# Optimization experiments

Hardware: AMD Instinct MI355X
Metric: run time of the kernel (lower is better)

## Reference

```python
import jax, jax.numpy as jnp
import numpy as np

B, L, D, H = 8, 1024, 512, 8
HD = D // H            # head_dim = 64
MAX_SEQ = 1024         # max_sequence_len
TEMP = 1.0


def setup_inputs() -> dict:
    key = jax.random.key(0)
    ks = jax.random.split(key, 9)
    w = lambda k, shape: jax.random.normal(k, shape, jnp.float32) * 0.02
    return {
        "x_q": jax.random.normal(ks[0], (B, L, D), jnp.float32),
        "x_k": jax.random.normal(ks[1], (B, L, D), jnp.float32),
        "x_v": jax.random.normal(ks[2], (B, L, D), jnp.float32),
        # causal mask: 1 where future (masked), 0 elsewhere; added as mask * -1e9
        "mask": jnp.triu(jnp.ones((L, L), jnp.float32), k=1),
        "Wq": w(ks[3], (D, D)), "bq": jnp.zeros((D,), jnp.float32),
        "Wk": w(ks[4], (D, D)), "bk": jnp.zeros((D,), jnp.float32),
        "Wv": w(ks[5], (D, D)), "bv": jnp.zeros((D,), jnp.float32),
        "Wo": w(ks[6], (D, D)), "bo": jnp.zeros((D,), jnp.float32),
        "rel_emb": w(ks[7], (MAX_SEQ, HD)),
    }


def _heads(x, W, b):
    # Dense + split heads: [B,L,D] -> [B,H,L,HD]
    y = x @ W + b
    Bx, Lx, _ = x.shape
    return y.reshape(Bx, Lx, H, HD).transpose(0, 2, 1, 3)


def reference(x_q, x_k, x_v, mask, Wq, bq, Wk, bk, Wv, bv, Wo, bo, rel_emb):
    Bx, Lq, Dx = x_q.shape
    Lk = x_k.shape[1]
    q = _heads(x_q, Wq, bq)   # [B,H,Lq,HD]
    k = _heads(x_k, Wk, bk)   # [B,H,Lk,HD]
    v = _heads(x_v, Wv, bv)   # [B,H,Lk,HD]

    scores = jnp.einsum('bhld,bhmd->bhlm', q, k)  # [B,H,Lq,Lk]

    # relative-position scores (Music Transformer skew trick)
    start = max(0, MAX_SEQ - Lq)
    E = rel_emb[start:]                              # [M,HD], M == Lq
    M = E.shape[0]
    rel = jnp.einsum('bhld,md->bhlm', q, E)          # [B,H,Lq,M]
    rel_mask = jnp.flip(jnp.tril(jnp.ones((Lq, M), jnp.float32)), axis=1)
    rel = rel * rel_mask
    # skew: pad one col on left, reshape swapping last two dims, drop first row
    padded = jnp.pad(rel, ((0, 0), (0, 0), (0, 0), (1, 0)))       # [B,H,Lq,M+1]
    skewed = padded.reshape(Bx, H, M + 1, Lq)[:, :, 1:, :]        # [B,H,M,Lq]
    skewed = skewed[:, :, :, :Lk]                                 # key_len <= query_len

    logits = (scores + skewed) / (jnp.sqrt(jnp.float32(HD)) * TEMP)
    logits = logits + mask * (-1e9)
    attn = jax.nn.softmax(logits, axis=-1)                        # [B,H,Lq,Lk]

    out = jnp.einsum('bhlm,bhmd->bhld', attn, v)                  # [B,H,Lq,HD]
    out = out.transpose(0, 2, 1, 3).reshape(Bx, Lq, Dx)
    out = out @ Wo + bo
    return out, attn
```

## Files before the change

### kernel.cpp

```cpp
#include <hip/hip_runtime.h>

typedef unsigned short u16;
typedef short bf8 __attribute__((ext_vector_type(8)));
typedef float f32x4 __attribute__((ext_vector_type(4)));

#define Bc 8
#define Hc 8
#define Lc 1024
#define Dc 512
#define HDc 64

__device__ __forceinline__ u16 f2bf(float f) {
    unsigned int x; __builtin_memcpy(&x, &f, 4);
    x = x + 0x7fffu + ((x >> 16) & 1u);
    return (u16)(x >> 16);
}
union S8 { bf8 v; u16 s[8]; };

__global__ __launch_bounds__(256) void relcvt(const float* __restrict__ src,
                                              u16* __restrict__ dst) {
    const int idx = blockIdx.x * 256 + threadIdx.x;
    const float4 v = *(const float4*)(src + (size_t)idx * 4);
    ushort4 o; o.x = f2bf(v.x); o.y = f2bf(v.y); o.z = f2bf(v.z); o.w = f2bf(v.w);
    *(ushort4*)(dst + (size_t)idx * 4) = o;
}

__global__ __launch_bounds__(256) void wtrans(
    const float* __restrict__ w0, const float* __restrict__ w1,
    const float* __restrict__ w2, const float* __restrict__ w3,
    u16* __restrict__ o0, u16* __restrict__ o1,
    u16* __restrict__ o2, u16* __restrict__ o3)
{
    const float* W; u16* O;
    switch (blockIdx.z) {
        case 0: W = w0; O = o0; break;
        case 1: W = w1; O = o1; break;
        case 2: W = w2; O = o2; break;
        default: W = w3; O = o3; break;
    }
    __shared__ float tile[64][65];
    const int t = threadIdx.x;
    const int k0 = blockIdx.x * 64, n0 = blockIdx.y * 64;
#pragma unroll
    for (int s = 0; s < 4; ++s) {
        const int idx = s * 256 + t;
        const int r = idx >> 4, c = (idx & 15) * 4;
        const float4 v = *(const float4*)(W + (size_t)(k0 + r) * Dc + n0 + c);
        tile[r][c] = v.x; tile[r][c + 1] = v.y; tile[r][c + 2] = v.z; tile[r][c + 3] = v.w;
    }
    __syncthreads();
#pragma unroll
    for (int s = 0; s < 2; ++s) {
        const int idx = s * 256 + t;
        const int rn = idx >> 3, ck = (idx & 7) * 8;
        S8 o;
#pragma unroll
        for (int u = 0; u < 8; ++u) o.s[u] = f2bf(tile[ck + u][rn]);
        *(bf8*)(O + (size_t)(n0 + rn) * Dc + k0 + ck) = o.v;
    }
}

__global__ __launch_bounds__(256) void gemm_mfma(
    const void* __restrict__ A, const u16* __restrict__ WT,
    const float* __restrict__ bias, void* __restrict__ Y,
    int aF32, int mode)
{
    __shared__ u16 As[128][72];
    __shared__ u16 Bs[64][72];

    const int t = threadIdx.x;
    const int w = t >> 6, lane = t & 63, quad = lane >> 4, l15 = lane & 15;
    const int m0 = blockIdx.x * 128, n0 = blockIdx.y * 64;

    f32x4 acc[2][4] = {};

    for (int k0 = 0; k0 < Dc; k0 += 64) {
#pragma unroll
        for (int s = 0; s < 4; ++s) {
            const int idx = s * 256 + t;
            const int r = idx >> 3, cb = (idx & 7) * 8;
            if (aF32) {
                const float* ap = (const float*)A + (size_t)(m0 + r) * Dc + k0 + cb;
                const float4 v0 = *(const float4*)ap;
                const float4 v1 = *(const float4*)(ap + 4);
                S8 o;
                o.s[0] = f2bf(v0.x); o.s[1] = f2bf(v0.y); o.s[2] = f2bf(v0.z); o.s[3] = f2bf(v0.w);
                o.s[4] = f2bf(v1.x); o.s[5] = f2bf(v1.y); o.s[6] = f2bf(v1.z); o.s[7] = f2bf(v1.w);
                *(bf8*)&As[r][cb] = o.v;
            } else {
                *(bf8*)&As[r][cb] = *(const bf8*)((const u16*)A + (size_t)(m0 + r) * Dc + k0 + cb);
            }
        }
#pragma unroll
        for (int s = 0; s < 2; ++s) {
            const int idx = s * 256 + t;
            const int r = idx >> 3, cb = (idx & 7) * 8;
            *(bf8*)&Bs[r][cb] = *(const bf8*)(WT + (size_t)(n0 + r) * Dc + k0 + cb);
        }
        __syncthreads();
#pragma unroll
        for (int ks = 0; ks < 2; ++ks) {
            const bf8 a0 = *(const bf8*)&As[w * 32 + l15][ks * 32 + quad * 8];
            const bf8 a1 = *(const bf8*)&As[w * 32 + 16 + l15][ks * 32 + quad * 8];
#pragma unroll
            for (int nt = 0; nt < 4; ++nt) {
                const bf8 b = *(const bf8*)&Bs[nt * 16 + l15][ks * 32 + quad * 8];
                acc[0][nt] = __builtin_amdgcn_mfma_f32_16x16x32_bf16(a0, b, acc[0][nt], 0, 0, 0);
                acc[1][nt] = __builtin_amdgcn_mfma_f32_16x16x32_bf16(a1, b, acc[1][nt], 0, 0, 0);
            }
        }
        __syncthreads();
    }

#pragma unroll
    for (int nt = 0; nt < 4; ++nt) {
        const int n = n0 + nt * 16 + l15;
        const float bv = bias[n];
#pragma unroll
        for (int mt = 0; mt < 2; ++mt) {
#pragma unroll
            for (int reg = 0; reg < 4; ++reg) {
                const int m = m0 + w * 32 + mt * 16 + quad * 4 + reg;
                const float val = acc[mt][nt][reg] + bv;
                if (mode == 0) {
                    ((float*)Y)[(size_t)m * Dc + n] = val;
                } else {
                    const int b = m >> 10, l = m & 1023;
                    const int h = n >> 6, hd = n & 63;
                    ((u16*)Y)[(((size_t)(b * Hc + h)) * Lc + l) * HDc + hd] = f2bf(val);
                }
            }
        }
    }
}

__global__ __launch_bounds__(256) void attn_mfma(
    const u16* __restrict__ q, const u16* __restrict__ k,
    const u16* __restrict__ v, const u16* __restrict__ rel,
    float* __restrict__ attn, u16* __restrict__ ows)
{
    __shared__ u16 kps[2][64][72];
    __shared__ u16 vst[2][64][72];
    __shared__ float rs[64][84];
    __shared__ float ls[64];

    const int bh = blockIdx.x;
    const int px = blockIdx.y;
    const int t = threadIdx.x;
    const int w = t >> 6, lane = t & 63, quad = lane >> 4, l15 = lane & 15;
    const int nt0 = 3 - w;
    const size_t qb = ((size_t)bh << 10);
    const int sr = t >> 3, scb = (t & 7) * 8;

    for (int seg = 0; seg < 2; ++seg) {
        const int it = seg ? (15 - px) : px;
        const int i0 = it * 64;

        __syncthreads();
        if (t < 64) ls[t] = 0.f;

        bf8 aq[2];
#pragma unroll
        for (int ks = 0; ks < 2; ++ks)
            aq[ks] = *(const bf8*)(q + (qb + i0 + w * 16 + l15) * HDc + ks * 32 + quad * 8);

        {
            const bf8 k0r = *(const bf8*)(k + (qb + sr) * HDc + scb);
            const bf8 k1r = *(const bf8*)(k + (qb + 32 + sr) * HDc + scb);
            *(bf8*)&kps[0][sr][scb] = k0r;
            *(bf8*)&kps[0][32 + sr][scb] = k1r;
        }
        int cur = 0;
        for (int jt = 0; jt <= it; ++jt) {
            const int j0 = jt * 64;
            const int mb = 960 - i0 + j0 + nt0 * 16;
            __syncthreads();
            const bool pf = (jt < it);
            bf8 kn0 = {}, kn1 = {};
            if (pf) {
                kn0 = *(const bf8*)(k + (qb + j0 + 64 + sr) * HDc + scb);
                kn1 = *(const bf8*)(k + (qb + j0 + 96 + sr) * HDc + scb);
            }

            f32x4 aS[4] = {}; f32x4 aR[5] = {};
#pragma unroll
            for (int ks = 0; ks < 2; ++ks) {
                const bf8 a = aq[ks];
#pragma unroll
                for (int nt = 0; nt < 4; ++nt) {
                    const bf8 b = *(const bf8*)&kps[cur][nt * 16 + l15][ks * 32 + quad * 8];
                    aS[nt] = __builtin_amdgcn_mfma_f32_16x16x32_bf16(a, b, aS[nt], 0, 0, 0);
                }
#pragma unroll
                for (int nt = 0; nt < 5; ++nt) {
                    int row = mb + nt * 16 + l15;
                    row = row > 1023 ? 1023 : row;
                    const bf8 b = *(const bf8*)(rel + (size_t)row * HDc + ks * 32 + quad * 8);
                    aR[nt] = __builtin_amdgcn_mfma_f32_16x16x32_bf16(a, b, aR[nt], 0, 0, 0);
                }
            }
#pragma unroll
            for (int nt = 0; nt < 5; ++nt)
#pragma unroll
                for (int reg = 0; reg < 4; ++reg)
                    rs[w * 16 + quad * 4 + reg][nt * 16 + l15] = aR[nt][reg];

            float psum[4] = {0.f, 0.f, 0.f, 0.f};
#pragma unroll
            for (int nt = 0; nt < 4; ++nt) {
#pragma unroll
                for (int reg = 0; reg < 4; ++reg) {
                    const int Rl = w * 16 + quad * 4 + reg;
                    const int cp = 15 - quad * 4 - reg + nt * 16 + l15;
                    const float sc = (aS[nt][reg] + rs[Rl][cp]) * 0.125f;
                    const bool valid = (j0 + nt * 16 + l15) <= (i0 + Rl);
                    psum[reg] += valid ? __expf(sc) : 0.f;
                }
            }
#pragma unroll
            for (int m = 1; m < 16; m <<= 1)
#pragma unroll
                for (int reg = 0; reg < 4; ++reg) psum[reg] += __shfl_xor(psum[reg], m, 64);
            if (l15 == 0) {
#pragma unroll
                for (int reg = 0; reg < 4; ++reg) ls[w * 16 + quad * 4 + reg] += psum[reg];
            }
            if (pf) {
                *(bf8*)&kps[cur ^ 1][sr][scb] = kn0;
                *(bf8*)&kps[cur ^ 1][32 + sr][scb] = kn1;
                cur ^= 1;
            }
        }

        __syncthreads();
        if (t < 64) ls[t] = 1.f / ls[t];

        f32x4 acc[4] = {};

        {
            const bf8 k0r = *(const bf8*)(k + (qb + sr) * HDc + scb);
            const bf8 k1r = *(const bf8*)(k + (qb + 32 + sr) * HDc + scb);
            S8 v0; v0.v = *(const bf8*)(v + (qb + sr) * HDc + scb);
            S8 v1; v1.v = *(const bf8*)(v + (qb + 32 + sr) * HDc + scb);
            *(bf8*)&kps[0][sr][scb] = k0r;
            *(bf8*)&kps[0][32 + sr][scb] = k1r;
            const int cp0 = (sr & 7) + 8 * (((sr >> 3) + (scb >> 3)) & 7);
            const int cp1 = (sr & 7) + 8 * ((4 + (sr >> 3) + (scb >> 3)) & 7);
#pragma unroll
            for (int u = 0; u < 8; ++u) vst[0][scb + u][cp0] = v0.s[u];
#pragma unroll
            for (int u = 0; u < 8; ++u) vst[0][scb + u][cp1] = v1.s[u];
        }
        cur = 0;
        for (int jt = 0; jt <= it; ++jt) {
            const int j0 = jt * 64;
            const int mb = 960 - i0 + j0 + nt0 * 16;
            __syncthreads();
            const bool pf = (jt < it);
            bf8 kn0 = {}, kn1 = {}, vn0 = {}, vn1 = {};
            if (pf) {
                kn0 = *(const bf8*)(k + (qb + j0 + 64 + sr) * HDc + scb);
                kn1 = *(const bf8*)(k + (qb + j0 + 96 + sr) * HDc + scb);
                vn0 = *(const bf8*)(v + (qb + j0 + 64 + sr) * HDc + scb);
                vn1 = *(const bf8*)(v + (qb + j0 + 96 + sr) * HDc + scb);
            }

            f32x4 aS[4] = {}; f32x4 aR[5] = {};
#pragma unroll
            for (int ks = 0; ks < 2; ++ks) {
                const bf8 a = aq[ks];
#pragma unroll
                for (int nt = 0; nt < 4; ++nt) {
                    const bf8 b = *(const bf8*)&kps[cur][nt * 16 + l15][ks * 32 + quad * 8];
                    aS[nt] = __builtin_amdgcn_mfma_f32_16x16x32_bf16(a, b, aS[nt], 0, 0, 0);
                }
#pragma unroll
                for (int nt = 0; nt < 5; ++nt) {
                    int row = mb + nt * 16 + l15;
                    row = row > 1023 ? 1023 : row;
                    const bf8 b = *(const bf8*)(rel + (size_t)row * HDc + ks * 32 + quad * 8);
                    aR[nt] = __builtin_amdgcn_mfma_f32_16x16x32_bf16(a, b, aR[nt], 0, 0, 0);
                }
            }
#pragma unroll
            for (int nt = 0; nt < 5; ++nt)
#pragma unroll
                for (int reg = 0; reg < 4; ++reg)
                    rs[w * 16 + quad * 4 + reg][nt * 16 + l15] = aR[nt][reg];

#pragma unroll
            for (int nt = 0; nt < 4; ++nt) {
                float pvv[4];
#pragma unroll
                for (int reg = 0; reg < 4; ++reg) {
                    const int Rl = w * 16 + quad * 4 + reg;
                    const int cp = 15 - quad * 4 - reg + nt * 16 + l15;
                    const float sc = (aS[nt][reg] + rs[Rl][cp]) * 0.125f;
                    const bool valid = (j0 + nt * 16 + l15) <= (i0 + Rl);
                    pvv[reg] = valid ? __expf(sc) * ls[Rl] : 0.f;
                }
                asm volatile("" ::: "memory");
#pragma unroll
                for (int reg = 0; reg < 4; ++reg) {
                    const int Rl = w * 16 + quad * 4 + reg;
                    attn[((size_t)bh * Lc + i0 + Rl) * Lc + j0 + nt * 16 + l15] = pvv[reg];
                    ((u16*)&rs[Rl][0])[nt * 16 + l15] = f2bf(pvv[reg]);
                }
            }

#pragma unroll
            for (int ks = 0; ks < 2; ++ks) {
                const bf8 pa = *(const bf8*)((const u16*)&rs[w * 16 + l15][0] + ks * 32 + quad * 8);
#pragma unroll
                for (int nt = 0; nt < 4; ++nt) {
                    const int d = nt * 16 + l15;
                    const bf8 vb = *(const bf8*)&vst[cur][d][8 * (((ks * 4 + quad) + (d >> 3)) & 7)];
                    acc[nt] = __builtin_amdgcn_mfma_f32_16x16x32_bf16(pa, vb, acc[nt], 0, 0, 0);
                }
            }

            if (pf) {
                *(bf8*)&kps[cur ^ 1][sr][scb] = kn0;
                *(bf8*)&kps[cur ^ 1][32 + sr][scb] = kn1;
                S8 a0; a0.v = vn0; S8 a1; a1.v = vn1;
                const int cp0 = (sr & 7) + 8 * (((sr >> 3) + (scb >> 3)) & 7);
                const int cp1 = (sr & 7) + 8 * ((4 + (sr >> 3) + (scb >> 3)) & 7);
#pragma unroll
                for (int u = 0; u < 8; ++u) vst[cur ^ 1][scb + u][cp0] = a0.s[u];
#pragma unroll
                for (int u = 0; u < 8; ++u) vst[cur ^ 1][scb + u][cp1] = a1.s[u];
                cur ^= 1;
            }
        }

        const int bb = bh >> 3, hh = bh & 7;
#pragma unroll
        for (int nt = 0; nt < 4; ++nt)
#pragma unroll
            for (int reg = 0; reg < 4; ++reg)
                ows[((size_t)(bb * Lc + i0 + w * 16 + quad * 4 + reg)) * Dc + hh * HDc + nt * 16 + l15]
                    = f2bf(acc[nt][reg]);

        const int jend = (it + 1) * 64;
        if (jend + t * 4 < Lc) {
            const float4 z = make_float4(0.f, 0.f, 0.f, 0.f);
            for (int r = 0; r < 64; ++r)
                *(float4*)(attn + ((size_t)bh * Lc + i0 + r) * Lc + jend + t * 4) = z;
        }
    }
}

extern "C" void kernel_launch(void* const* d_in, const int* in_sizes, int n_in,
                              void* d_out, int out_size, void* d_ws, size_t ws_size,
                              hipStream_t stream)
{
    const float* x_q = (const float*)d_in[0];
    const float* x_k = (const float*)d_in[1];
    const float* x_v = (const float*)d_in[2];
    const float* Wq = (const float*)d_in[4];
    const float* bq = (const float*)d_in[5];
    const float* Wk = (const float*)d_in[6];
    const float* bk = (const float*)d_in[7];
    const float* Wv = (const float*)d_in[8];
    const float* bv = (const float*)d_in[9];
    const float* Wo = (const float*)d_in[10];
    const float* bo = (const float*)d_in[11];
    const float* rel = (const float*)d_in[12];

    float* out  = (float*)d_out;
    float* attn = out + (size_t)Bc * Lc * Dc;

    u16* relbf = (u16*)d_ws;
    u16* wqT = relbf + (size_t)1024 * 64;
    u16* wkT = wqT + (size_t)Dc * Dc;
    u16* wvT = wkT + (size_t)Dc * Dc;
    u16* woT = wvT + (size_t)Dc * Dc;
    u16* qbf = woT + (size_t)Dc * Dc;
    u16* kbf = qbf + (size_t)Bc * Lc * Dc;
    u16* vbf = kbf + (size_t)Bc * Lc * Dc;
    u16* owsbf = vbf + (size_t)Bc * Lc * Dc;

    relcvt<<<64, 256, 0, stream>>>(rel, relbf);
    wtrans<<<dim3(8, 8, 4), 256, 0, stream>>>(Wq, Wk, Wv, Wo, wqT, wkT, wvT, woT);

    dim3 gg(64, 8);
    gemm_mfma<<<gg, 256, 0, stream>>>(x_q, wqT, bq, qbf, 1, 1);
    gemm_mfma<<<gg, 256, 0, stream>>>(x_k, wkT, bk, kbf, 1, 1);
    gemm_mfma<<<gg, 256, 0, stream>>>(x_v, wvT, bv, vbf, 1, 1);

    attn_mfma<<<dim3(64, 8), 256, 0, stream>>>(qbf, kbf, vbf, relbf, attn, owsbf);

    gemm_mfma<<<gg, 256, 0, stream>>>(owsbf, woT, bo, out, 0, 0);
}
```

Before: 549.1 us.

## Double-buffer GEMM with XCD-aware tiling and coalesced nontemporal attention stores

```diff
diff --git a/kernel.cpp b/kernel.cpp
--- a/kernel.cpp
+++ b/kernel.cpp
@@ -65,51 +65,81 @@
     const float* __restrict__ bias, void* __restrict__ Y,
     int aF32, int mode)
 {
-    __shared__ u16 As[128][72];
-    __shared__ u16 Bs[64][72];
+    __shared__ u16 As[2][64][72];
+    __shared__ u16 Bs[2][64][72];
+
+    const int wgid = blockIdx.x;
+    const int xcd = wgid & 7, rr = wgid >> 3;
+    const int mt = xcd + 8 * (rr >> 3), ntile = rr & 7;
+    const int m0 = mt * 64, n0 = ntile * 64;
 
     const int t = threadIdx.x;
     const int w = t >> 6, lane = t & 63, quad = lane >> 4, l15 = lane & 15;
-    const int m0 = blockIdx.x * 128, n0 = blockIdx.y * 64;
-
-    f32x4 acc[2][4] = {};
-
+    const int ra = t >> 2, ca = (t & 3) * 16;
+
+    f32x4 acc[4] = {};
+
+    {
+        S8 o0, o1;
+        if (aF32) {
+            const float* ap = (const float*)A + (size_t)(m0 + ra) * Dc + ca;
+            const float4 v0 = *(const float4*)ap,       v1 = *(const float4*)(ap + 4);
+            const float4 v2 = *(const float4*)(ap + 8), v3 = *(const float4*)(ap + 12);
+            o0.s[0] = f2bf(v0.x); o0.s[1] = f2bf(v0.y); o0.s[2] = f2bf(v0.z); o0.s[3] = f2bf(v0.w);
+            o0.s[4] = f2bf(v1.x); o0.s[5] = f2bf(v1.y); o0.s[6] = f2bf(v1.z); o0.s[7] = f2bf(v1.w);
+            o1.s[0] = f2bf(v2.x); o1.s[1] = f2bf(v2.y); o1.s[2] = f2bf(v2.z); o1.s[3] = f2bf(v2.w);
+            o1.s[4] = f2bf(v3.x); o1.s[5] = f2bf(v3.y); o1.s[6] = f2bf(v3.z); o1.s[7] = f2bf(v3.w);
+        } else {
+            const u16* ap = (const u16*)A + (size_t)(m0 + ra) * Dc + ca;
+            o0.v = *(const bf8*)ap; o1.v = *(const bf8*)(ap + 8);
+        }
+        *(bf8*)&As[0][ra][ca] = o0.v; *(bf8*)&As[0][ra][ca + 8] = o1.v;
+        const u16* bp = WT + (size_t)(n0 + ra) * Dc + ca;
+        *(bf8*)&Bs[0][ra][ca] = *(const bf8*)bp;
+        *(bf8*)&Bs[0][ra][ca + 8] = *(const bf8*)(bp + 8);
+    }
+
+    int cur = 0;
     for (int k0 = 0; k0 < Dc; k0 += 64) {
-#pragma unroll
-        for (int s = 0; s < 4; ++s) {
-            const int idx = s * 256 + t;
-            const int r = idx >> 3, cb = (idx & 7) * 8;
+        __syncthreads();
+        const bool pf = (k0 + 64 < Dc);
+        float4 v0, v1, v2, v3; bf8 an0 = {}, an1 = {}, bn0 = {}, bn1 = {};
+        if (pf) {
+            const int kn = k0 + 64;
             if (aF32) {
-                const float* ap = (const float*)A + (size_t)(m0 + r) * Dc + k0 + cb;
-                const float4 v0 = *(const float4*)ap;
-                const float4 v1 = *(const float4*)(ap + 4);
-                S8 o;
-                o.s[0] = f2bf(v0.x); o.s[1] = f2bf(v0.y); o.s[2] = f2bf(v0.z); o.s[3] = f2bf(v0.w);
-                o.s[4] = f2bf(v1.x); o.s[5] = f2bf(v1.y); o.s[6] = f2bf(v1.z); o.s[7] = f2bf(v1.w);
-                *(bf8*)&As[r][cb] = o.v;
+                const float* ap = (const float*)A + (size_t)(m0 + ra) * Dc + kn + ca;
+                v0 = *(const float4*)ap;       v1 = *(const float4*)(ap + 4);
+                v2 = *(const float4*)(ap + 8); v3 = *(const float4*)(ap + 12);
             } else {
-                *(bf8*)&As[r][cb] = *(const bf8*)((const u16*)A + (size_t)(m0 + r) * Dc + k0 + cb);
-            }
-        }
-#pragma unroll
-        for (int s = 0; s < 2; ++s) {
-            const int idx = s * 256 + t;
-            const int r = idx >> 3, cb = (idx & 7) * 8;
-            *(bf8*)&Bs[r][cb] = *(const bf8*)(WT + (size_t)(n0 + r) * Dc + k0 + cb);
-        }
-        __syncthreads();
+                const u16* ap = (const u16*)A + (size_t)(m0 + ra) * Dc + kn + ca;
+                an0 = *(const bf8*)ap; an1 = *(const bf8*)(ap + 8);
+            }
+            const u16* bp = WT + (size_t)(n0 + ra) * Dc + kn + ca;
+            bn0 = *(const bf8*)bp; bn1 = *(const bf8*)(bp + 8);
+        }
+
 #pragma unroll
         for (int ks = 0; ks < 2; ++ks) {
-            const bf8 a0 = *(const bf8*)&As[w * 32 + l15][ks * 32 + quad * 8];
-            const bf8 a1 = *(const bf8*)&As[w * 32 + 16 + l15][ks * 32 + quad * 8];
+            const bf8 a = *(const bf8*)&As[cur][w * 16 + l15][ks * 32 + quad * 8];
 #pragma unroll
             for (int nt = 0; nt < 4; ++nt) {
-                const bf8 b = *(const bf8*)&Bs[nt * 16 + l15][ks * 32 + quad * 8];
-                acc[0][nt] = __builtin_amdgcn_mfma_f32_16x16x32_bf16(a0, b, acc[0][nt], 0, 0, 0);
-                acc[1][nt] = __builtin_amdgcn_mfma_f32_16x16x32_bf16(a1, b, acc[1][nt], 0, 0, 0);
-            }
-        }
-        __syncthreads();
+                const bf8 b = *(const bf8*)&Bs[cur][nt * 16 + l15][ks * 32 + quad * 8];
+                acc[nt] = __builtin_amdgcn_mfma_f32_16x16x32_bf16(a, b, acc[nt], 0, 0, 0);
+            }
+        }
+
+        if (pf) {
+            S8 o0, o1;
+            if (aF32) {
+                o0.s[0] = f2bf(v0.x); o0.s[1] = f2bf(v0.y); o0.s[2] = f2bf(v0.z); o0.s[3] = f2bf(v0.w);
+                o0.s[4] = f2bf(v1.x); o0.s[5] = f2bf(v1.y); o0.s[6] = f2bf(v1.z); o0.s[7] = f2bf(v1.w);
+                o1.s[0] = f2bf(v2.x); o1.s[1] = f2bf(v2.y); o1.s[2] = f2bf(v2.z); o1.s[3] = f2bf(v2.w);
+                o1.s[4] = f2bf(v3.x); o1.s[5] = f2bf(v3.y); o1.s[6] = f2bf(v3.z); o1.s[7] = f2bf(v3.w);
+            } else { o0.v = an0; o1.v = an1; }
+            *(bf8*)&As[cur ^ 1][ra][ca] = o0.v; *(bf8*)&As[cur ^ 1][ra][ca + 8] = o1.v;
+            *(bf8*)&Bs[cur ^ 1][ra][ca] = bn0;  *(bf8*)&Bs[cur ^ 1][ra][ca + 8] = bn1;
+            cur ^= 1;
+        }
     }
 
 #pragma unroll
@@ -117,18 +147,15 @@
         const int n = n0 + nt * 16 + l15;
         const float bv = bias[n];
 #pragma unroll
-        for (int mt = 0; mt < 2; ++mt) {
-#pragma unroll
-            for (int reg = 0; reg < 4; ++reg) {
-                const int m = m0 + w * 32 + mt * 16 + quad * 4 + reg;
-                const float val = acc[mt][nt][reg] + bv;
-                if (mode == 0) {
-                    ((float*)Y)[(size_t)m * Dc + n] = val;
-                } else {
-                    const int b = m >> 10, l = m & 1023;
-                    const int h = n >> 6, hd = n & 63;
-                    ((u16*)Y)[(((size_t)(b * Hc + h)) * Lc + l) * HDc + hd] = f2bf(val);
-                }
+        for (int reg = 0; reg < 4; ++reg) {
+            const int m = m0 + w * 16 + quad * 4 + reg;
+            const float val = acc[nt][reg] + bv;
+            if (mode == 0) {
+                __builtin_nontemporal_store(val, (float*)Y + (size_t)m * Dc + n);
+            } else {
+                const int b = m >> 10, l = m & 1023;
+                const int h = n >> 6, hd = n & 63;
+                ((u16*)Y)[(((size_t)(b * Hc + h)) * Lc + l) * HDc + hd] = f2bf(val);
             }
         }
     }
@@ -141,7 +168,7 @@
 {
     __shared__ u16 kps[2][64][72];
     __shared__ u16 vst[2][64][72];
-    __shared__ float rs[64][84];
+    __shared__ float rs[64][96];
     __shared__ float ls[64];
 
     const int bh = blockIdx.x;
@@ -288,23 +315,26 @@
                 for (int reg = 0; reg < 4; ++reg)
                     rs[w * 16 + quad * 4 + reg][nt * 16 + l15] = aR[nt][reg];
 
+            float pvv[4][4];
 #pragma unroll
             for (int nt = 0; nt < 4; ++nt) {
-                float pvv[4];
 #pragma unroll
                 for (int reg = 0; reg < 4; ++reg) {
                     const int Rl = w * 16 + quad * 4 + reg;
                     const int cp = 15 - quad * 4 - reg + nt * 16 + l15;
                     const float sc = (aS[nt][reg] + rs[Rl][cp]) * 0.125f;
                     const bool valid = (j0 + nt * 16 + l15) <= (i0 + Rl);
-                    pvv[reg] = valid ? __expf(sc) * ls[Rl] : 0.f;
-                }
-                asm volatile("" ::: "memory");
+                    pvv[nt][reg] = valid ? __expf(sc) * ls[Rl] : 0.f;
+                }
+            }
+            asm volatile("" ::: "memory");
+#pragma unroll
+            for (int nt = 0; nt < 4; ++nt) {
 #pragma unroll
                 for (int reg = 0; reg < 4; ++reg) {
                     const int Rl = w * 16 + quad * 4 + reg;
-                    attn[((size_t)bh * Lc + i0 + Rl) * Lc + j0 + nt * 16 + l15] = pvv[reg];
-                    ((u16*)&rs[Rl][0])[nt * 16 + l15] = f2bf(pvv[reg]);
+                    ((u16*)&rs[Rl][0])[nt * 16 + l15] = f2bf(pvv[nt][reg]);
+                    rs[Rl][32 + nt * 16 + l15] = pvv[nt][reg];
                 }
             }
 
@@ -331,6 +361,15 @@
                 for (int u = 0; u < 8; ++u) vst[cur ^ 1][scb + u][cp1] = a1.s[u];
                 cur ^= 1;
             }
+
+            __syncthreads();
+            const int trow = t >> 4, tcol = (t & 15) * 4;
+#pragma unroll
+            for (int s = 0; s < 4; ++s) {
+                const f32x4 p4 = *(const f32x4*)&rs[trow + 16 * s][32 + tcol];
+                __builtin_nontemporal_store(p4,
+                    (f32x4*)(attn + ((size_t)bh * Lc + i0 + trow + 16 * s) * Lc + j0 + tcol));
+            }
         }
 
         const int bb = bh >> 3, hh = bh & 7;
@@ -343,9 +382,10 @@
 
         const int jend = (it + 1) * 64;
         if (jend + t * 4 < Lc) {
-            const float4 z = make_float4(0.f, 0.f, 0.f, 0.f);
+            const f32x4 z = {0.f, 0.f, 0.f, 0.f};
             for (int r = 0; r < 64; ++r)
-                *(float4*)(attn + ((size_t)bh * Lc + i0 + r) * Lc + jend + t * 4) = z;
+                __builtin_nontemporal_store(z,
+                    (f32x4*)(attn + ((size_t)bh * Lc + i0 + r) * Lc + jend + t * 4));
         }
     }
 }
@@ -383,12 +423,11 @@
     relcvt<<<64, 256, 0, stream>>>(rel, relbf);
     wtrans<<<dim3(8, 8, 4), 256, 0, stream>>>(Wq, Wk, Wv, Wo, wqT, wkT, wvT, woT);
 
-    dim3 gg(64, 8);
-    gemm_mfma<<<gg, 256, 0, stream>>>(x_q, wqT, bq, qbf, 1, 1);
-    gemm_mfma<<<gg, 256, 0, stream>>>(x_k, wkT, bk, kbf, 1, 1);
-    gemm_mfma<<<gg, 256, 0, stream>>>(x_v, wvT, bv, vbf, 1, 1);
+    gemm_mfma<<<1024, 256, 0, stream>>>(x_q, wqT, bq, qbf, 1, 1);
+    gemm_mfma<<<1024, 256, 0, stream>>>(x_k, wkT, bk, kbf, 1, 1);
+    gemm_mfma<<<1024, 256, 0, stream>>>(x_v, wvT, bv, vbf, 1, 1);
 
     attn_mfma<<<dim3(64, 8), 256, 0, stream>>>(qbf, kbf, vbf, relbf, attn, owsbf);
 
-    gemm_mfma<<<gg, 256, 0, stream>>>(owsbf, woT, bo, out, 0, 0);
-}
+    gemm_mfma<<<1024, 256, 0, stream>>>(owsbf, woT, bo, out, 0, 0);
+}
```

Measured after the change: 469.8 us. -14.4%, faster.

## Double-buffer GEMM tiles, XCD-aware block mapping, shuffle-based rel skew, coalesced attn stores

Applied to the files above, without the earlier changes.

```diff
diff --git a/kernel.cpp b/kernel.cpp
--- a/kernel.cpp
+++ b/kernel.cpp
@@ -65,65 +65,111 @@
     const float* __restrict__ bias, void* __restrict__ Y,
     int aF32, int mode)
 {
-    __shared__ u16 As[128][72];
-    __shared__ u16 Bs[64][72];
+    __shared__ u16 As[2][128][72];
+    __shared__ u16 Bs[2][64][72];
+
+    const int wgid = blockIdx.x;
+    const int xcd = wgid & 7, rr = wgid >> 3;
+    const int mt = xcd * 8 + (rr >> 3), ntl = rr & 7;
+    const int m0 = mt * 128, n0 = ntl * 64;
 
     const int t = threadIdx.x;
     const int w = t >> 6, lane = t & 63, quad = lane >> 4, l15 = lane & 15;
-    const int m0 = blockIdx.x * 128, n0 = blockIdx.y * 64;
 
     f32x4 acc[2][4] = {};
 
-    for (int k0 = 0; k0 < Dc; k0 += 64) {
+    {
 #pragma unroll
         for (int s = 0; s < 4; ++s) {
-            const int idx = s * 256 + t;
-            const int r = idx >> 3, cb = (idx & 7) * 8;
+            const int idx = s * 256 + t, r = idx >> 3, cb = (idx & 7) * 8;
+            S8 o;
             if (aF32) {
-                const float* ap = (const float*)A + (size_t)(m0 + r) * Dc + k0 + cb;
-                const float4 v0 = *(const float4*)ap;
-                const float4 v1 = *(const float4*)(ap + 4);
-                S8 o;
+                const float* ap = (const float*)A + (size_t)(m0 + r) * Dc + cb;
+                const float4 v0 = *(const float4*)ap, v1 = *(const float4*)(ap + 4);
                 o.s[0] = f2bf(v0.x); o.s[1] = f2bf(v0.y); o.s[2] = f2bf(v0.z); o.s[3] = f2bf(v0.w);
                 o.s[4] = f2bf(v1.x); o.s[5] = f2bf(v1.y); o.s[6] = f2bf(v1.z); o.s[7] = f2bf(v1.w);
-                *(bf8*)&As[r][cb] = o.v;
             } else {
-                *(bf8*)&As[r][cb] = *(const bf8*)((const u16*)A + (size_t)(m0 + r) * Dc + k0 + cb);
-            }
+                o.v = *(const bf8*)((const u16*)A + (size_t)(m0 + r) * Dc + cb);
+            }
+            *(bf8*)&As[0][r][cb] = o.v;
         }
 #pragma unroll
         for (int s = 0; s < 2; ++s) {
-            const int idx = s * 256 + t;
-            const int r = idx >> 3, cb = (idx & 7) * 8;
-            *(bf8*)&Bs[r][cb] = *(const bf8*)(WT + (size_t)(n0 + r) * Dc + k0 + cb);
-        }
+            const int idx = s * 256 + t, r = idx >> 3, cb = (idx & 7) * 8;
+            *(bf8*)&Bs[0][r][cb] = *(const bf8*)(WT + (size_t)(n0 + r) * Dc + cb);
+        }
+    }
+
+    int cur = 0;
+    for (int k0 = 0; k0 < Dc; k0 += 64) {
         __syncthreads();
+        const bool pf = (k0 + 64 < Dc);
+        float4 fv[4][2]; bf8 av[4] = {}; bf8 bv[2] = {};
+        if (pf) {
+            const int kn = k0 + 64;
+#pragma unroll
+            for (int s = 0; s < 4; ++s) {
+                const int idx = s * 256 + t, r = idx >> 3, cb = (idx & 7) * 8;
+                if (aF32) {
+                    const float* ap = (const float*)A + (size_t)(m0 + r) * Dc + kn + cb;
+                    fv[s][0] = *(const float4*)ap; fv[s][1] = *(const float4*)(ap + 4);
+                } else {
+                    av[s] = *(const bf8*)((const u16*)A + (size_t)(m0 + r) * Dc + kn + cb);
+                }
+            }
+#pragma unroll
+            for (int s = 0; s < 2; ++s) {
+                const int idx = s * 256 + t, r = idx >> 3, cb = (idx & 7) * 8;
+                bv[s] = *(const bf8*)(WT + (size_t)(n0 + r) * Dc + kn + cb);
+            }
+        }
+
 #pragma unroll
         for (int ks = 0; ks < 2; ++ks) {
-            const bf8 a0 = *(const bf8*)&As[w * 32 + l15][ks * 32 + quad * 8];
-            const bf8 a1 = *(const bf8*)&As[w * 32 + 16 + l15][ks * 32 + quad * 8];
+            const bf8 a0 = *(const bf8*)&As[cur][w * 32 + l15][ks * 32 + quad * 8];
+            const bf8 a1 = *(const bf8*)&As[cur][w * 32 + 16 + l15][ks * 32 + quad * 8];
 #pragma unroll
             for (int nt = 0; nt < 4; ++nt) {
-                const bf8 b = *(const bf8*)&Bs[nt * 16 + l15][ks * 32 + quad * 8];
+                const bf8 b = *(const bf8*)&Bs[cur][nt * 16 + l15][ks * 32 + quad * 8];
                 acc[0][nt] = __builtin_amdgcn_mfma_f32_16x16x32_bf16(a0, b, acc[0][nt], 0, 0, 0);
                 acc[1][nt] = __builtin_amdgcn_mfma_f32_16x16x32_bf16(a1, b, acc[1][nt], 0, 0, 0);
             }
         }
-        __syncthreads();
+
+        if (pf) {
+#pragma unroll
+            for (int s = 0; s < 4; ++s) {
+                const int idx = s * 256 + t, r = idx >> 3, cb = (idx & 7) * 8;
+                S8 o;
+                if (aF32) {
+                    o.s[0] = f2bf(fv[s][0].x); o.s[1] = f2bf(fv[s][0].y);
+                    o.s[2] = f2bf(fv[s][0].z); o.s[3] = f2bf(fv[s][0].w);
+                    o.s[4] = f2bf(fv[s][1].x); o.s[5] = f2bf(fv[s][1].y);
+                    o.s[6] = f2bf(fv[s][1].z); o.s[7] = f2bf(fv[s][1].w);
+                } else { o.v = av[s]; }
+                *(bf8*)&As[cur ^ 1][r][cb] = o.v;
+            }
+#pragma unroll
+            for (int s = 0; s < 2; ++s) {
+                const int idx = s * 256 + t, r = idx >> 3, cb = (idx & 7) * 8;
+                *(bf8*)&Bs[cur ^ 1][r][cb] = bv[s];
+            }
+            cur ^= 1;
+        }
     }
 
 #pragma unroll
     for (int nt = 0; nt < 4; ++nt) {
         const int n = n0 + nt * 16 + l15;
-        const float bv = bias[n];
-#pragma unroll
-        for (int mt = 0; mt < 2; ++mt) {
+        const float bv2 = bias[n];
+#pragma unroll
+        for (int mi = 0; mi < 2; ++mi) {
 #pragma unroll
             for (int reg = 0; reg < 4; ++reg) {
-                const int m = m0 + w * 32 + mt * 16 + quad * 4 + reg;
-                const float val = acc[mt][nt][reg] + bv;
+                const int m = m0 + w * 32 + mi * 16 + quad * 4 + reg;
+                const float val = acc[mi][nt][reg] + bv2;
                 if (mode == 0) {
-                    ((float*)Y)[(size_t)m * Dc + n] = val;
+                    __builtin_nontemporal_store(val, (float*)Y + (size_t)m * Dc + n);
                 } else {
                     const int b = m >> 10, l = m & 1023;
                     const int h = n >> 6, hd = n & 63;
@@ -141,7 +187,8 @@
 {
     __shared__ u16 kps[2][64][72];
     __shared__ u16 vst[2][64][72];
-    __shared__ float rs[64][84];
+    __shared__ u16 p16[64][72];
+    __shared__ float p32[64][68];
     __shared__ float ls[64];
 
     const int bh = blockIdx.x;
@@ -151,6 +198,14 @@
     const int nt0 = 3 - w;
     const size_t qb = ((size_t)bh << 10);
     const int sr = t >> 3, scb = (t & 7) * 8;
+
+    int sl[4]; bool cy[4];
+#pragma unroll
+    for (int reg = 0; reg < 4; ++reg) {
+        const int s = l15 + 15 - (quad * 4 + reg);
+        sl[reg] = (quad << 4) | (s & 15);
+        cy[reg] = s >= 16;
+    }
 
     for (int seg = 0; seg < 2; ++seg) {
         const int it = seg ? (15 - px) : px;
@@ -199,11 +254,13 @@
                     aR[nt] = __builtin_amdgcn_mfma_f32_16x16x32_bf16(a, b, aR[nt], 0, 0, 0);
                 }
             }
-#pragma unroll
-            for (int nt = 0; nt < 5; ++nt)
+
+            float g[5][4];
+#pragma unroll
+            for (int m = 0; m < 5; ++m)
 #pragma unroll
                 for (int reg = 0; reg < 4; ++reg)
-                    rs[w * 16 + quad * 4 + reg][nt * 16 + l15] = aR[nt][reg];
+                    g[m][reg] = __shfl(aR[m][reg], sl[reg], 64);
 
             float psum[4] = {0.f, 0.f, 0.f, 0.f};
 #pragma unroll
@@ -211,8 +268,8 @@
 #pragma unroll
                 for (int reg = 0; reg < 4; ++reg) {
                     const int Rl = w * 16 + quad * 4 + reg;
-                    const int cp = 15 - quad * 4 - reg + nt * 16 + l15;
-                    const float sc = (aS[nt][reg] + rs[Rl][cp]) * 0.125f;
+                    const float relv = cy[reg] ? g[nt + 1][reg] : g[nt][reg];
+                    const float sc = (aS[nt][reg] + relv) * 0.125f;
                     const bool valid = (j0 + nt * 16 + l15) <= (i0 + Rl);
                     psum[reg] += valid ? __expf(sc) : 0.f;
                 }
@@ -282,35 +339,36 @@
                     aR[nt] = __builtin_amdgcn_mfma_f32_16x16x32_bf16(a, b, aR[nt], 0, 0, 0);
                 }
             }
-#pragma unroll
-            for (int nt = 0; nt < 5; ++nt)
+
+            float g[5][4];
+#pragma unroll
+            for (int m = 0; m < 5; ++m)
 #pragma unroll
                 for (int reg = 0; reg < 4; ++reg)
-                    rs[w * 16 + quad * 4 + reg][nt * 16 + l15] = aR[nt][reg];
+                    g[m][reg] = __shfl(aR[m][reg], sl[reg], 64);
+
+            float ils[4];
+#pragma unroll
+            for (int reg = 0; reg < 4; ++reg) ils[reg] = ls[w * 16 + quad * 4 + reg];
 
 #pragma unroll
             for (int nt = 0; nt < 4; ++nt) {
-                float pvv[4];
 #pragma unroll
                 for (int reg = 0; reg < 4; ++reg) {
                     const int Rl = w * 16 + quad * 4 + reg;
-                    const int cp = 15 - quad * 4 - reg + nt * 16 + l15;
-                    const float sc = (aS[nt][reg] + rs[Rl][cp]) * 0.125f;
+                    const float relv = cy[reg] ? g[nt + 1][reg] : g[nt][reg];
+                    const float sc = (aS[nt][reg] + relv) * 0.125f;
                     const bool valid = (j0 + nt * 16 + l15) <= (i0 + Rl);
-                    pvv[reg] = valid ? __expf(sc) * ls[Rl] : 0.f;
-                }
-                asm volatile("" ::: "memory");
-#pragma unroll
-                for (int reg = 0; reg < 4; ++reg) {
-                    const int Rl = w * 16 + quad * 4 + reg;
-                    attn[((size_t)bh * Lc + i0 + Rl) * Lc + j0 + nt * 16 + l15] = pvv[reg];
-                    ((u16*)&rs[Rl][0])[nt * 16 + l15] = f2bf(pvv[reg]);
-                }
-            }
+                    const float p = valid ? __expf(sc) * ils[reg] : 0.f;
+                    p16[Rl][nt * 16 + l15] = f2bf(p);
+                    p32[Rl][nt * 16 + l15] = p;
+                }
+            }
+            asm volatile("" ::: "memory");
 
 #pragma unroll
             for (int ks = 0; ks < 2; ++ks) {
-                const bf8 pa = *(const bf8*)((const u16*)&rs[w * 16 + l15][0] + ks * 32 + quad * 8);
+                const bf8 pa = *(const bf8*)((const u16*)&p16[w * 16 + l15][0] + ks * 32 + quad * 8);
 #pragma unroll
                 for (int nt = 0; nt < 4; ++nt) {
                     const int d = nt * 16 + l15;
@@ -331,6 +389,15 @@
                 for (int u = 0; u < 8; ++u) vst[cur ^ 1][scb + u][cp1] = a1.s[u];
                 cur ^= 1;
             }
+
+            __syncthreads();
+            const int trow = t >> 4, tcol = (t & 15) * 4;
+#pragma unroll
+            for (int s = 0; s < 4; ++s) {
+                const f32x4 p4 = *(const f32x4*)&p32[trow + 16 * s][tcol];
+                __builtin_nontemporal_store(p4,
+                    (f32x4*)(attn + ((size_t)bh * Lc + i0 + trow + 16 * s) * Lc + j0 + tcol));
+            }
         }
 
         const int bb = bh >> 3, hh = bh & 7;
@@ -343,9 +410,10 @@
 
         const int jend = (it + 1) * 64;
         if (jend + t * 4 < Lc) {
-            const float4 z = make_float4(0.f, 0.f, 0.f, 0.f);
+            const f32x4 z = {0.f, 0.f, 0.f, 0.f};
             for (int r = 0; r < 64; ++r)
-                *(float4*)(attn + ((size_t)bh * Lc + i0 + r) * Lc + jend + t * 4) = z;
+                __builtin_nontemporal_store(z,
+                    (f32x4*)(attn + ((size_t)bh * Lc + i0 + r) * Lc + jend + t * 4));
         }
     }
 }
@@ -383,12 +451,11 @@
     relcvt<<<64, 256, 0, stream>>>(rel, relbf);
     wtrans<<<dim3(8, 8, 4), 256, 0, stream>>>(Wq, Wk, Wv, Wo, wqT, wkT, wvT, woT);
 
-    dim3 gg(64, 8);
-    gemm_mfma<<<gg, 256, 0, stream>>>(x_q, wqT, bq, qbf, 1, 1);
-    gemm_mfma<<<gg, 256, 0, stream>>>(x_k, wkT, bk, kbf, 1, 1);
-    gemm_mfma<<<gg, 256, 0, stream>>>(x_v, wvT, bv, vbf, 1, 1);
+    gemm_mfma<<<512, 256, 0, stream>>>(x_q, wqT, bq, qbf, 1, 1);
+    gemm_mfma<<<512, 256, 0, stream>>>(x_k, wkT, bk, kbf, 1, 1);
+    gemm_mfma<<<512, 256, 0, stream>>>(x_v, wvT, bv, vbf, 1, 1);
 
     attn_mfma<<<dim3(64, 8), 256, 0, stream>>>(qbf, kbf, vbf, relbf, attn, owsbf);
 
-    gemm_mfma<<<gg, 256, 0, stream>>>(owsbf, woT, bo, out, 0, 0);
-}
+    gemm_mfma<<<512, 256, 0, stream>>>(owsbf, woT, bo, out, 0, 0);
+}
```

New measurement: 591.7 us. 7.8% more time.
